# Optimization experiments

Hardware: AMD Instinct MI355X
Metric: run time of the kernel (lower is better)

## Reference

```python
import jax, jax.numpy as jnp
import numpy as np

B, D, K, H, E, Z = 64, 25000, 16, 128, 256, 32


def setup_inputs() -> dict:
    key = jax.random.key(0)
    ks = jax.random.split(key, 10)
    s = 0.02
    return {
        "x": jax.random.normal(ks[0], (B, D), jnp.float32),
        "mask": jax.random.randint(ks[1], (B, D), 0, 2, jnp.int32),
        "feat_emb": jax.random.normal(ks[2], (D, K), jnp.float32),          # feature_embedding [D,K]
        "feat_bias": jnp.zeros((D, 1), jnp.float32),                        # feature_bias [D,1]
        "W1": jax.random.normal(ks[3], (1 + K + 1, H), jnp.float32) * s,    # h_layer linear 1 (in,out)
        "b1": jnp.zeros((H,), jnp.float32),
        "W2": jax.random.normal(ks[4], (H, K), jnp.float32) * s,            # h_layer linear 2
        "b2": jnp.zeros((K,), jnp.float32),
        "We1": jax.random.normal(ks[5], (K, E), jnp.float32) * s,           # encoder_mlp linear 1
        "be1": jnp.zeros((E,), jnp.float32),
        "We2": jax.random.normal(ks[6], (E, 2 * Z), jnp.float32) * s,       # encoder_mlp linear 2
        "be2": jnp.zeros((2 * Z,), jnp.float32),
    }


def reference(x, mask, feat_emb, feat_bias, W1, b1, W2, b2, We1, be1, We2, be2):
    b, d = x.shape
    k = feat_emb.shape[1]
    # Build per-(sample, feature) input rows: [x_bd, F_d(K), bias_d] -> [B, D, 1+K+1]
    h_in = jnp.concatenate(
        [
            x[:, :, None],
            jnp.broadcast_to(feat_emb[None, :, :], (b, d, k)),
            jnp.broadcast_to(feat_bias[None, :, :], (b, d, 1)),
        ],
        axis=-1,
    )
    # Shared small MLP (h_layer), dropout is identity at rate 0.0
    h = jax.nn.relu(h_in @ W1 + b1)          # [B, D, H]
    h = jax.nn.relu(h @ W2 + b2)             # [B, D, K]
    # Masked sum pooling over features
    c = jnp.sum(h * mask.astype(h.dtype)[:, :, None], axis=1)  # [B, K]
    # encoder_mlp
    enc = jax.nn.relu(c @ We1 + be1) @ We2 + be2                # [B, 2Z]
    mu, logvar = jnp.split(enc, 2, axis=-1)
    return mu, logvar
```

## Files before the change

kernel.cpp:

```cpp
#include <hip/hip_runtime.h>
#include <hip/hip_bf16.h>

#define B 64
#define D 25000
#define K 16
#define H 128
#define E 256
#define Z 32
#define DTILE 10
#define NBLK (D / DTILE)
#define NREP 8
#define MSTR 68

#define REP_BYTES (NREP * B * K * 4)
#define HI_OFF    REP_BYTES
#define W1F_OFF   (HI_OFF + H * K * 2)

typedef __attribute__((ext_vector_type(8))) _Float16 half8;
typedef __attribute__((ext_vector_type(2))) _Float16 hv2;
typedef __attribute__((ext_vector_type(4))) float f32x4;

__global__ __launch_bounds__(256) void prep_kernel(
    const float* __restrict__ W1, const float* __restrict__ b1,
    const float* __restrict__ W2, float* __restrict__ rep,
    _Float16* __restrict__ hiW2, _Float16* __restrict__ w1f)
{
    const int t = threadIdx.x;
    const int bid = blockIdx.x;
    if (bid < NREP) {
        for (int i = t; i < B * K; i += 256) rep[bid * B * K + i] = 0.f;
    } else if (bid == NREP) {
        for (int i = t; i < H * K; i += 256) {
            int j = i & 7, n = (i >> 3) & 15, g = (i >> 7) & 3, s = i >> 9;
            int k = s * 32 + g * 8 + j;
            hiW2[i] = (_Float16)W2[k * K + n];
        }
    } else {
        for (int i = t; i < 8 * 64 * 8; i += 256) {
            int j = i & 7, lane = (i >> 3) & 63, c = i >> 9;
            int g = lane >> 4, n = lane & 15;
            int k = g * 8 + j;
            int h = c * 16 + n;
            float v;
            if (k < 16)       v = W1[(1 + k) * H + h];
            else if (k == 16) v = W1[17 * H + h];
            else if (k == 17) v = b1[h];
            else              v = 0.f;
            w1f[i] = (_Float16)v;
        }
    }
}

__global__ __launch_bounds__(256) void partial_main_kernel(
    const float* __restrict__ x, const int* __restrict__ mask,
    const float* __restrict__ feat_emb, const float* __restrict__ feat_bias,
    const float* __restrict__ W1, const float* __restrict__ b2,
    const _Float16* __restrict__ hiW2, const _Float16* __restrict__ w1f,
    float* __restrict__ rep)
{
    __shared__ __align__(16) _Float16 sGh[DTILE * H];
    __shared__ __align__(16) float sMf[DTILE * MSTR];

    const int t    = threadIdx.x;
    const int d0   = blockIdx.x * DTILE;
    const int lane = t & 63;
    const int wv   = t >> 6;
    const int g    = lane >> 4;
    const int n    = lane & 15;

    for (int i = t; i < DTILE * B; i += 256) {
        int bb = i / DTILE, dd = i - bb * DTILE;
        sMf[dd * MSTR + bb] = (float)mask[bb * D + d0 + dd];
    }

    {
        const int m  = n;
        const int dA = min(d0 + m, D - 1);
        union AF { half8 v; _Float16 e[8]; } af;
        if (g < 2) {
            const float4* fe = (const float4*)&feat_emb[(size_t)dA * K + g * 8];
            float4 u0 = fe[0], u1 = fe[1];
            af.e[0] = (_Float16)u0.x; af.e[1] = (_Float16)u0.y;
            af.e[2] = (_Float16)u0.z; af.e[3] = (_Float16)u0.w;
            af.e[4] = (_Float16)u1.x; af.e[5] = (_Float16)u1.y;
            af.e[6] = (_Float16)u1.z; af.e[7] = (_Float16)u1.w;
        } else if (g == 2) {
            af.e[0] = (_Float16)feat_bias[dA];
            af.e[1] = (_Float16)1.f;
            #pragma unroll
            for (int j = 2; j < 8; ++j) af.e[j] = (_Float16)0.f;
        } else {
            #pragma unroll
            for (int j = 0; j < 8; ++j) af.e[j] = (_Float16)0.f;
        }
        #pragma unroll
        for (int cc = 0; cc < 2; ++cc) {
            const int c = wv * 2 + cc;
            half8 bf = *(const half8*)(w1f + (((c << 6) + lane) << 3));
            f32x4 C = {0.f, 0.f, 0.f, 0.f};
            C = __builtin_amdgcn_mfma_f32_16x16x32_f16(af.v, bf, C, 0, 0, 0);
            #pragma unroll
            for (int r = 0; r < 4; ++r) {
                const int m2 = g * 4 + r;
                if (m2 < DTILE) sGh[m2 * H + c * 16 + n] = (_Float16)C[r];
            }
        }
    }

    const float* xrow = x + (size_t)(wv * 16 + n) * D + d0;
    hv2 xh[DTILE / 2];
    #pragma unroll
    for (int i = 0; i < DTILE / 2; ++i) {
        float2 xv = *(const float2*)(xrow + 2 * i);
        xh[i] = (hv2){(_Float16)xv.x, (_Float16)xv.y};
    }

    half8 Bf[4];
    #pragma unroll
    for (int s = 0; s < 4; ++s)
        Bf[s] = *(const half8*)(hiW2 + (((s * 4 + g) * 16 + n) << 3));
    hv2 w0h[4][4];
    #pragma unroll
    for (int s = 0; s < 4; ++s) {
        const float4* wp = (const float4*)&W1[s * 32 + g * 8];
        float4 a0 = wp[0], a1 = wp[1];
        w0h[s][0] = (hv2){(_Float16)a0.x, (_Float16)a0.y};
        w0h[s][1] = (hv2){(_Float16)a0.z, (_Float16)a0.w};
        w0h[s][2] = (hv2){(_Float16)a1.x, (_Float16)a1.y};
        w0h[s][3] = (hv2){(_Float16)a1.z, (_Float16)a1.w};
    }
    const float b2n = b2[n];
    const hv2 zeroh = {(_Float16)0.f, (_Float16)0.f};
    __syncthreads();

    f32x4 cacc = {0.f, 0.f, 0.f, 0.f};
    const int moff = wv * 16 + g * 4;
    const _Float16* gb0 = sGh + g * 8;

    #pragma unroll
    for (int i = 0; i < DTILE / 2; ++i) {
        const int dd0 = 2 * i, dd1 = 2 * i + 1;
        const hv2 xa = {xh[i].x, xh[i].x};
        const hv2 xb = {xh[i].y, xh[i].y};
        f32x4 c1a = {b2n, b2n, b2n, b2n};
        f32x4 c1b = {b2n, b2n, b2n, b2n};
        #pragma unroll
        for (int s = 0; s < 4; ++s) {
            union GA { half8 v; hv2 p[4]; };
            GA ga, gb, A0, A1;
            ga.v = *(const half8*)(gb0 + dd0 * H + s * 32);
            gb.v = *(const half8*)(gb0 + dd1 * H + s * 32);
            #pragma unroll
            for (int p = 0; p < 4; ++p) {
                hv2 h0 = __builtin_elementwise_fma(xa, w0h[s][p], ga.p[p]);
                hv2 h1 = __builtin_elementwise_fma(xb, w0h[s][p], gb.p[p]);
                A0.p[p] = __builtin_elementwise_max(h0, zeroh);
                A1.p[p] = __builtin_elementwise_max(h1, zeroh);
            }
            c1a = __builtin_amdgcn_mfma_f32_16x16x32_f16(A0.v, Bf[s], c1a, 0, 0, 0);
            c1b = __builtin_amdgcn_mfma_f32_16x16x32_f16(A1.v, Bf[s], c1b, 0, 0, 0);
        }
        const float4 mv0 = *(const float4*)&sMf[dd0 * MSTR + moff];
        const float4 mv1 = *(const float4*)&sMf[dd1 * MSTR + moff];
        cacc[0] = fmaf(mv0.x, fmaxf(c1a[0], 0.f), fmaf(mv1.x, fmaxf(c1b[0], 0.f), cacc[0]));
        cacc[1] = fmaf(mv0.y, fmaxf(c1a[1], 0.f), fmaf(mv1.y, fmaxf(c1b[1], 0.f), cacc[1]));
        cacc[2] = fmaf(mv0.z, fmaxf(c1a[2], 0.f), fmaf(mv1.z, fmaxf(c1b[2], 0.f), cacc[2]));
        cacc[3] = fmaf(mv0.w, fmaxf(c1a[3], 0.f), fmaf(mv1.w, fmaxf(c1b[3], 0.f), cacc[3]));
    }

    float* crep = rep + (size_t)(blockIdx.x & (NREP - 1)) * (B * K);
    #pragma unroll
    for (int r = 0; r < 4; ++r)
        atomicAdd(&crep[(moff + r) * K + n], cacc[r]);
}

__global__ __launch_bounds__(256) void partial_enc_kernel(
    const float* __restrict__ rep, const float* __restrict__ We1,
    const float* __restrict__ be1, const float* __restrict__ We2,
    const float* __restrict__ be2, float* __restrict__ out)
{
    const int b = blockIdx.x;
    const int t = threadIdx.x;
    __shared__ float sc[K];
    __shared__ float st1[E];
    __shared__ float red[256];

    {
        const int k = t & 15, grp = t >> 4;
        red[t] = (grp < NREP) ? rep[grp * (B * K) + b * K + k] : 0.f;
    }
    __syncthreads();
    if (t < K) {
        float s2 = 0.f;
        #pragma unroll
        for (int q = 0; q < 16; ++q) s2 += red[q * 16 + t];
        sc[t] = s2;
    }
    __syncthreads();

    {
        float acc = be1[t];
        #pragma unroll
        for (int k = 0; k < K; ++k)
            acc = fmaf(sc[k], We1[k * E + t], acc);
        st1[t] = fmaxf(acc, 0.f);
    }
    __syncthreads();

    const int j = t & 63, seg = t >> 6;
    float acc = 0.f;
    #pragma unroll 4
    for (int e = seg * 64; e < seg * 64 + 64; ++e)
        acc = fmaf(st1[e], We2[e * 64 + j], acc);
    red[t] = acc;
    __syncthreads();

    if (t < 64) {
        float v = red[j] + red[64 + j] + red[128 + j] + red[192 + j] + be2[j];
        if (j < Z) out[b * Z + j] = v;
        else       out[B * Z + b * Z + (j - Z)] = v;
    }
}

extern "C" void kernel_launch(void* const* d_in, const int* in_sizes, int n_in,
                              void* d_out, int out_size, void* d_ws, size_t ws_size,
                              hipStream_t stream) {
    const float* x         = (const float*)d_in[0];
    const int*   mask      = (const int*)  d_in[1];
    const float* feat_emb  = (const float*)d_in[2];
    const float* feat_bias = (const float*)d_in[3];
    const float* W1        = (const float*)d_in[4];
    const float* b1        = (const float*)d_in[5];
    const float* W2        = (const float*)d_in[6];
    const float* b2        = (const float*)d_in[7];
    const float* We1       = (const float*)d_in[8];
    const float* be1       = (const float*)d_in[9];
    const float* We2       = (const float*)d_in[10];
    const float* be2       = (const float*)d_in[11];

    float*     rep  = (float*)d_ws;
    _Float16*  hiW2 = (_Float16*)((char*)d_ws + HI_OFF);
    _Float16*  w1f  = (_Float16*)((char*)d_ws + W1F_OFF);

    prep_kernel<<<NREP + 2, 256, 0, stream>>>(W1, b1, W2, rep, hiW2, w1f);
    partial_main_kernel<<<NBLK, 256, 0, stream>>>(
        x, mask, feat_emb, feat_bias, W1, b2, hiW2, w1f, rep);
    partial_enc_kernel<<<B, 256, 0, stream>>>(
        rep, We1, be1, We2, be2, (float*)d_out);
}
```

Before: 113.2 us.

## Pre-transpose x and mask to fp16 D-major layout in prep kernel

Adds a transpose stage to the prep kernel that converts x and mask from [B,D] fp32/int32 into [D,B] fp16 buffers in workspace. The main kernel then loads each tile's x and mask contiguously into shared memory, instead of doing strided per-sample loads across rows of length D. This targets the poorly coalesced gathers in the main kernel. In exchange it adds a full extra pass that reads x and mask and writes the fp16 copies, and it rounds the mask to fp16, which is exact for 0/1 values.

```diff
diff --git a/kernel.cpp b/kernel.cpp
--- a/kernel.cpp
+++ b/kernel.cpp
@@ -10,20 +10,25 @@
 #define DTILE 10
 #define NBLK (D / DTILE)
 #define NREP 8
-#define MSTR 68
+#define NTILE ((D + 63) / 64)
 
 #define REP_BYTES (NREP * B * K * 4)
 #define HI_OFF    REP_BYTES
 #define W1F_OFF   (HI_OFF + H * K * 2)
+#define XT_OFF    (W1F_OFF + 8 * 64 * 8 * 2)
+#define MT_OFF    (XT_OFF + D * B * 2)
 
 typedef __attribute__((ext_vector_type(8))) _Float16 half8;
+typedef __attribute__((ext_vector_type(4))) _Float16 hv4;
 typedef __attribute__((ext_vector_type(2))) _Float16 hv2;
 typedef __attribute__((ext_vector_type(4))) float f32x4;
 
 __global__ __launch_bounds__(256) void prep_kernel(
+    const float* __restrict__ x, const int* __restrict__ mask,
     const float* __restrict__ W1, const float* __restrict__ b1,
     const float* __restrict__ W2, float* __restrict__ rep,
-    _Float16* __restrict__ hiW2, _Float16* __restrict__ w1f)
+    _Float16* __restrict__ hiW2, _Float16* __restrict__ w1f,
+    _Float16* __restrict__ xTh, _Float16* __restrict__ mTh)
 {
     const int t = threadIdx.x;
     const int bid = blockIdx.x;
@@ -35,12 +40,11 @@
             int k = s * 32 + g * 8 + j;
             hiW2[i] = (_Float16)W2[k * K + n];
         }
-    } else {
+    } else if (bid == NREP + 1) {
         for (int i = t; i < 8 * 64 * 8; i += 256) {
             int j = i & 7, lane = (i >> 3) & 63, c = i >> 9;
             int g = lane >> 4, n = lane & 15;
-            int k = g * 8 + j;
-            int h = c * 16 + n;
+            int k = g * 8 + j, h = c * 16 + n;
             float v;
             if (k < 16)       v = W1[(1 + k) * H + h];
             else if (k == 16) v = W1[17 * H + h];
@@ -48,18 +52,37 @@
             else              v = 0.f;
             w1f[i] = (_Float16)v;
         }
+    } else {
+        __shared__ float tx[64 * 65];
+        __shared__ float tm[64 * 65];
+        const int dt0 = (bid - NREP - 2) * 64;
+        const int dn  = min(64, D - dt0);
+        for (int i = t; i < 64 * 64; i += 256) {
+            int bb = i >> 6, dd = i & 63;
+            if (dd < dn) {
+                tx[dd * 65 + bb] = x[(size_t)bb * D + dt0 + dd];
+                tm[dd * 65 + bb] = (float)mask[(size_t)bb * D + dt0 + dd];
+            }
+        }
+        __syncthreads();
+        for (int i = t; i < dn * 64; i += 256) {
+            int dd = i >> 6, bb = i & 63;
+            xTh[(size_t)(dt0 + dd) * 64 + bb] = (_Float16)tx[dd * 65 + bb];
+            mTh[(size_t)(dt0 + dd) * 64 + bb] = (_Float16)tm[dd * 65 + bb];
+        }
     }
 }
 
 __global__ __launch_bounds__(256) void partial_main_kernel(
-    const float* __restrict__ x, const int* __restrict__ mask,
     const float* __restrict__ feat_emb, const float* __restrict__ feat_bias,
     const float* __restrict__ W1, const float* __restrict__ b2,
     const _Float16* __restrict__ hiW2, const _Float16* __restrict__ w1f,
+    const _Float16* __restrict__ xTh, const _Float16* __restrict__ mTh,
     float* __restrict__ rep)
 {
     __shared__ __align__(16) _Float16 sGh[DTILE * H];
-    __shared__ __align__(16) float sMf[DTILE * MSTR];
+    __shared__ __align__(16) _Float16 sXh[DTILE * B];
+    __shared__ __align__(16) _Float16 sMh[DTILE * B];
 
     const int t    = threadIdx.x;
     const int d0   = blockIdx.x * DTILE;
@@ -68,9 +91,12 @@
     const int g    = lane >> 4;
     const int n    = lane & 15;
 
-    for (int i = t; i < DTILE * B; i += 256) {
-        int bb = i / DTILE, dd = i - bb * DTILE;
-        sMf[dd * MSTR + bb] = (float)mask[bb * D + d0 + dd];
+    {
+        const unsigned* xs = (const unsigned*)(xTh + (size_t)d0 * B);
+        const unsigned* ms = (const unsigned*)(mTh + (size_t)d0 * B);
+        unsigned* xd = (unsigned*)sXh;
+        unsigned* md = (unsigned*)sMh;
+        for (int i = t; i < DTILE * B / 2; i += 256) { xd[i] = xs[i]; md[i] = ms[i]; }
     }
 
     {
@@ -107,14 +133,6 @@
         }
     }
 
-    const float* xrow = x + (size_t)(wv * 16 + n) * D + d0;
-    hv2 xh[DTILE / 2];
-    #pragma unroll
-    for (int i = 0; i < DTILE / 2; ++i) {
-        float2 xv = *(const float2*)(xrow + 2 * i);
-        xh[i] = (hv2){(_Float16)xv.x, (_Float16)xv.y};
-    }
-
     half8 Bf[4];
     #pragma unroll
     for (int s = 0; s < 4; ++s)
@@ -132,6 +150,12 @@
     const float b2n = b2[n];
     const hv2 zeroh = {(_Float16)0.f, (_Float16)0.f};
     __syncthreads();
+
+    const int sample = wv * 16 + n;
+    hv2 xh[DTILE / 2];
+    #pragma unroll
+    for (int i = 0; i < DTILE / 2; ++i)
+        xh[i] = (hv2){sXh[(2 * i) * B + sample], sXh[(2 * i + 1) * B + sample]};
 
     f32x4 cacc = {0.f, 0.f, 0.f, 0.f};
     const int moff = wv * 16 + g * 4;
@@ -160,12 +184,12 @@
             c1a = __builtin_amdgcn_mfma_f32_16x16x32_f16(A0.v, Bf[s], c1a, 0, 0, 0);
             c1b = __builtin_amdgcn_mfma_f32_16x16x32_f16(A1.v, Bf[s], c1b, 0, 0, 0);
         }
-        const float4 mv0 = *(const float4*)&sMf[dd0 * MSTR + moff];
-        const float4 mv1 = *(const float4*)&sMf[dd1 * MSTR + moff];
-        cacc[0] = fmaf(mv0.x, fmaxf(c1a[0], 0.f), fmaf(mv1.x, fmaxf(c1b[0], 0.f), cacc[0]));
-        cacc[1] = fmaf(mv0.y, fmaxf(c1a[1], 0.f), fmaf(mv1.y, fmaxf(c1b[1], 0.f), cacc[1]));
-        cacc[2] = fmaf(mv0.z, fmaxf(c1a[2], 0.f), fmaf(mv1.z, fmaxf(c1b[2], 0.f), cacc[2]));
-        cacc[3] = fmaf(mv0.w, fmaxf(c1a[3], 0.f), fmaf(mv1.w, fmaxf(c1b[3], 0.f), cacc[3]));
+        hv4 m0 = *(const hv4*)&sMh[dd0 * B + moff];
+        hv4 m1 = *(const hv4*)&sMh[dd1 * B + moff];
+        cacc[0] = fmaf((float)m0.x, fmaxf(c1a[0], 0.f), fmaf((float)m1.x, fmaxf(c1b[0], 0.f), cacc[0]));
+        cacc[1] = fmaf((float)m0.y, fmaxf(c1a[1], 0.f), fmaf((float)m1.y, fmaxf(c1b[1], 0.f), cacc[1]));
+        cacc[2] = fmaf((float)m0.z, fmaxf(c1a[2], 0.f), fmaf((float)m1.z, fmaxf(c1b[2], 0.f), cacc[2]));
+        cacc[3] = fmaf((float)m0.w, fmaxf(c1a[3], 0.f), fmaf((float)m1.w, fmaxf(c1b[3], 0.f), cacc[3]));
     }
 
     float* crep = rep + (size_t)(blockIdx.x & (NREP - 1)) * (B * K);
@@ -241,10 +265,13 @@
     float*     rep  = (float*)d_ws;
     _Float16*  hiW2 = (_Float16*)((char*)d_ws + HI_OFF);
     _Float16*  w1f  = (_Float16*)((char*)d_ws + W1F_OFF);
-
-    prep_kernel<<<NREP + 2, 256, 0, stream>>>(W1, b1, W2, rep, hiW2, w1f);
+    _Float16*  xTh  = (_Float16*)((char*)d_ws + XT_OFF);
+    _Float16*  mTh  = (_Float16*)((char*)d_ws + MT_OFF);
+
+    prep_kernel<<<NREP + 2 + NTILE, 256, 0, stream>>>(
+        x, mask, W1, b1, W2, rep, hiW2, w1f, xTh, mTh);
     partial_main_kernel<<<NBLK, 256, 0, stream>>>(
-        x, mask, feat_emb, feat_bias, W1, b2, hiW2, w1f, rep);
+        feat_emb, feat_bias, W1, b2, hiW2, w1f, xTh, mTh, rep);
     partial_enc_kernel<<<B, 256, 0, stream>>>(
         rep, We1, be1, We2, be2, (float*)d_out);
 }
```

Result: no change. 112.8 us, median of 2 (-0.3%).

## Pre-transpose mask to fp16 and give each wave its own layer-1 tile

Applied to the files above, without the earlier changes.

Adds a prep pass that transposes the int32 mask into a [D,B] fp16 buffer, so the main kernel loads per-lane mask values straight from global memory instead of doing strided gathers into shared memory. Each wave now computes the full feature-dependent layer-1 term into its own shared buffer, which removes the block-wide __syncthreads at the cost of four times the redundant MFMA work and shared memory. The extra prep blocks add a read and write of the mask array before the main kernel runs.

```diff
diff --git a/kernel.cpp b/kernel.cpp
--- a/kernel.cpp
+++ b/kernel.cpp
@@ -10,20 +10,23 @@
 #define DTILE 10
 #define NBLK (D / DTILE)
 #define NREP 8
-#define MSTR 68
+#define NTILE ((D + 63) / 64)
 
 #define REP_BYTES (NREP * B * K * 4)
 #define HI_OFF    REP_BYTES
 #define W1F_OFF   (HI_OFF + H * K * 2)
+#define MT_OFF    (W1F_OFF + 8 * 64 * 8 * 2)
 
 typedef __attribute__((ext_vector_type(8))) _Float16 half8;
+typedef __attribute__((ext_vector_type(4))) _Float16 hv4;
 typedef __attribute__((ext_vector_type(2))) _Float16 hv2;
 typedef __attribute__((ext_vector_type(4))) float f32x4;
 
 __global__ __launch_bounds__(256) void prep_kernel(
-    const float* __restrict__ W1, const float* __restrict__ b1,
-    const float* __restrict__ W2, float* __restrict__ rep,
-    _Float16* __restrict__ hiW2, _Float16* __restrict__ w1f)
+    const int* __restrict__ mask, const float* __restrict__ W1,
+    const float* __restrict__ b1, const float* __restrict__ W2,
+    float* __restrict__ rep, _Float16* __restrict__ hiW2,
+    _Float16* __restrict__ w1f, _Float16* __restrict__ mTh)
 {
     const int t = threadIdx.x;
     const int bid = blockIdx.x;
@@ -35,12 +38,11 @@
             int k = s * 32 + g * 8 + j;
             hiW2[i] = (_Float16)W2[k * K + n];
         }
-    } else {
+    } else if (bid == NREP + 1) {
         for (int i = t; i < 8 * 64 * 8; i += 256) {
             int j = i & 7, lane = (i >> 3) & 63, c = i >> 9;
             int g = lane >> 4, n = lane & 15;
-            int k = g * 8 + j;
-            int h = c * 16 + n;
+            int k = g * 8 + j, h = c * 16 + n;
             float v;
             if (k < 16)       v = W1[(1 + k) * H + h];
             else if (k == 16) v = W1[17 * H + h];
@@ -48,18 +50,30 @@
             else              v = 0.f;
             w1f[i] = (_Float16)v;
         }
+    } else {
+        __shared__ float tm[64 * 65];
+        const int dt0 = (bid - NREP - 2) * 64;
+        const int dn  = min(64, D - dt0);
+        for (int i = t; i < 64 * 64; i += 256) {
+            int bb = i >> 6, dd = i & 63;
+            if (dd < dn) tm[dd * 65 + bb] = (float)mask[(size_t)bb * D + dt0 + dd];
+        }
+        __syncthreads();
+        for (int i = t; i < dn * 64; i += 256) {
+            int dd = i >> 6, bb = i & 63;
+            mTh[(size_t)(dt0 + dd) * 64 + bb] = (_Float16)tm[dd * 65 + bb];
+        }
     }
 }
 
 __global__ __launch_bounds__(256) void partial_main_kernel(
-    const float* __restrict__ x, const int* __restrict__ mask,
-    const float* __restrict__ feat_emb, const float* __restrict__ feat_bias,
-    const float* __restrict__ W1, const float* __restrict__ b2,
-    const _Float16* __restrict__ hiW2, const _Float16* __restrict__ w1f,
+    const float* __restrict__ x, const float* __restrict__ feat_emb,
+    const float* __restrict__ feat_bias, const float* __restrict__ W1,
+    const float* __restrict__ b2, const _Float16* __restrict__ hiW2,
+    const _Float16* __restrict__ w1f, const _Float16* __restrict__ mTh,
     float* __restrict__ rep)
 {
-    __shared__ __align__(16) _Float16 sGh[DTILE * H];
-    __shared__ __align__(16) float sMf[DTILE * MSTR];
+    __shared__ __align__(16) _Float16 sG4[4][DTILE * H];
 
     const int t    = threadIdx.x;
     const int d0   = blockIdx.x * DTILE;
@@ -67,25 +81,21 @@
     const int wv   = t >> 6;
     const int g    = lane >> 4;
     const int n    = lane & 15;
-
-    for (int i = t; i < DTILE * B; i += 256) {
-        int bb = i / DTILE, dd = i - bb * DTILE;
-        sMf[dd * MSTR + bb] = (float)mask[bb * D + d0 + dd];
-    }
+    _Float16* sGw  = sG4[wv];
 
     {
-        const int m  = n;
-        const int dA = min(d0 + m, D - 1);
+        const int dA = d0 + n;
+        const int dAc = min(dA, D - 1);
         union AF { half8 v; _Float16 e[8]; } af;
         if (g < 2) {
-            const float4* fe = (const float4*)&feat_emb[(size_t)dA * K + g * 8];
+            const float4* fe = (const float4*)&feat_emb[(size_t)dAc * K + g * 8];
             float4 u0 = fe[0], u1 = fe[1];
             af.e[0] = (_Float16)u0.x; af.e[1] = (_Float16)u0.y;
             af.e[2] = (_Float16)u0.z; af.e[3] = (_Float16)u0.w;
             af.e[4] = (_Float16)u1.x; af.e[5] = (_Float16)u1.y;
             af.e[6] = (_Float16)u1.z; af.e[7] = (_Float16)u1.w;
         } else if (g == 2) {
-            af.e[0] = (_Float16)feat_bias[dA];
+            af.e[0] = (_Float16)feat_bias[dAc];
             af.e[1] = (_Float16)1.f;
             #pragma unroll
             for (int j = 2; j < 8; ++j) af.e[j] = (_Float16)0.f;
@@ -94,26 +104,32 @@
             for (int j = 0; j < 8; ++j) af.e[j] = (_Float16)0.f;
         }
         #pragma unroll
-        for (int cc = 0; cc < 2; ++cc) {
-            const int c = wv * 2 + cc;
+        for (int c = 0; c < 8; ++c) {
             half8 bf = *(const half8*)(w1f + (((c << 6) + lane) << 3));
             f32x4 C = {0.f, 0.f, 0.f, 0.f};
             C = __builtin_amdgcn_mfma_f32_16x16x32_f16(af.v, bf, C, 0, 0, 0);
             #pragma unroll
             for (int r = 0; r < 4; ++r) {
                 const int m2 = g * 4 + r;
-                if (m2 < DTILE) sGh[m2 * H + c * 16 + n] = (_Float16)C[r];
+                if (m2 < DTILE) sGw[m2 * H + c * 16 + n] = (_Float16)C[r];
             }
         }
     }
 
-    const float* xrow = x + (size_t)(wv * 16 + n) * D + d0;
+    const int sample = wv * 16 + n;
+    const int moff   = wv * 16 + g * 4;
+
+    const float* xrow = x + (size_t)sample * D + d0;
     hv2 xh[DTILE / 2];
     #pragma unroll
     for (int i = 0; i < DTILE / 2; ++i) {
         float2 xv = *(const float2*)(xrow + 2 * i);
         xh[i] = (hv2){(_Float16)xv.x, (_Float16)xv.y};
     }
+    hv4 mv[DTILE];
+    #pragma unroll
+    for (int dd = 0; dd < DTILE; ++dd)
+        mv[dd] = *(const hv4*)(mTh + (size_t)(d0 + dd) * B + moff);
 
     half8 Bf[4];
     #pragma unroll
@@ -131,11 +147,9 @@
     }
     const float b2n = b2[n];
     const hv2 zeroh = {(_Float16)0.f, (_Float16)0.f};
-    __syncthreads();
 
     f32x4 cacc = {0.f, 0.f, 0.f, 0.f};
-    const int moff = wv * 16 + g * 4;
-    const _Float16* gb0 = sGh + g * 8;
+    const _Float16* gb0 = sGw + g * 8;
 
     #pragma unroll
     for (int i = 0; i < DTILE / 2; ++i) {
@@ -160,12 +174,10 @@
             c1a = __builtin_amdgcn_mfma_f32_16x16x32_f16(A0.v, Bf[s], c1a, 0, 0, 0);
             c1b = __builtin_amdgcn_mfma_f32_16x16x32_f16(A1.v, Bf[s], c1b, 0, 0, 0);
         }
-        const float4 mv0 = *(const float4*)&sMf[dd0 * MSTR + moff];
-        const float4 mv1 = *(const float4*)&sMf[dd1 * MSTR + moff];
-        cacc[0] = fmaf(mv0.x, fmaxf(c1a[0], 0.f), fmaf(mv1.x, fmaxf(c1b[0], 0.f), cacc[0]));
-        cacc[1] = fmaf(mv0.y, fmaxf(c1a[1], 0.f), fmaf(mv1.y, fmaxf(c1b[1], 0.f), cacc[1]));
-        cacc[2] = fmaf(mv0.z, fmaxf(c1a[2], 0.f), fmaf(mv1.z, fmaxf(c1b[2], 0.f), cacc[2]));
-        cacc[3] = fmaf(mv0.w, fmaxf(c1a[3], 0.f), fmaf(mv1.w, fmaxf(c1b[3], 0.f), cacc[3]));
+        cacc[0] = fmaf((float)mv[dd0].x, fmaxf(c1a[0], 0.f), fmaf((float)mv[dd1].x, fmaxf(c1b[0], 0.f), cacc[0]));
+        cacc[1] = fmaf((float)mv[dd0].y, fmaxf(c1a[1], 0.f), fmaf((float)mv[dd1].y, fmaxf(c1b[1], 0.f), cacc[1]));
+        cacc[2] = fmaf((float)mv[dd0].z, fmaxf(c1a[2], 0.f), fmaf((float)mv[dd1].z, fmaxf(c1b[2], 0.f), cacc[2]));
+        cacc[3] = fmaf((float)mv[dd0].w, fmaxf(c1a[3], 0.f), fmaf((float)mv[dd1].w, fmaxf(c1b[3], 0.f), cacc[3]));
     }
 
     float* crep = rep + (size_t)(blockIdx.x & (NREP - 1)) * (B * K);
@@ -241,10 +253,12 @@
     float*     rep  = (float*)d_ws;
     _Float16*  hiW2 = (_Float16*)((char*)d_ws + HI_OFF);
     _Float16*  w1f  = (_Float16*)((char*)d_ws + W1F_OFF);
-
-    prep_kernel<<<NREP + 2, 256, 0, stream>>>(W1, b1, W2, rep, hiW2, w1f);
+    _Float16*  mTh  = (_Float16*)((char*)d_ws + MT_OFF);
+
+    prep_kernel<<<NREP + 2 + NTILE, 256, 0, stream>>>(
+        mask, W1, b1, W2, rep, hiW2, w1f, mTh);
     partial_main_kernel<<<NBLK, 256, 0, stream>>>(
-        x, mask, feat_emb, feat_bias, W1, b2, hiW2, w1f, rep);
+        x, feat_emb, feat_bias, W1, b2, hiW2, w1f, mTh, rep);
     partial_enc_kernel<<<B, 256, 0, stream>>>(
         rep, We1, be1, We2, be2, (float*)d_out);
 }
```

New measurement: 122.6 us. +8.3%, slower.
